# Optimization experiments

Measured on AMD Instinct MI355X. Metric: run time of the kernel, lower is better.

Reference implementation:

```python
import jax, jax.numpy as jnp
from jax import lax
import numpy as np
import math

B, L, UNITS, DM, P = 2048, 2, 16, 512, 16
CH = UNITS // P            # 1  (attention 'head' dim c)
D = DM // P                # 32
C_ATT = CH * D             # 32 channels in patch space
C_FFN = 4 * C_ATT          # 128
HALF = P // 2              # 8 (post-stride-2 patch size)
EPS = 1e-5


def _to_patches(x):
    # 'b (c p1) (d p2) -> b (c d) p1 p2'
    b = x.shape[0]
    x = x.reshape(b, CH, P, D, P).transpose(0, 1, 3, 2, 4)
    return x.reshape(b, CH * D, P, P)


def _from_patches(x):
    # 'b (c d) p1 p2 -> b (c p1) (d p2)'
    b = x.shape[0]
    x = x.reshape(b, CH, D, P, P).transpose(0, 1, 3, 2, 4)
    return x.reshape(b, CH * P, D * P)


def _layernorm(x, g, b):
    m = jnp.mean(x, -1, keepdims=True)
    v = jnp.mean((x - m) ** 2, -1, keepdims=True)
    return (x - m) * lax.rsqrt(v + EPS) * g + b


def _dw_block(x, dw_w, dw_b, bn_g, bn_b, bn_m, bn_v, pw_w, pw_b, stride):
    # depthwise 3x3 conv -> BatchNorm (eval) -> 1x1 pointwise conv
    C = x.shape[1]
    y = lax.conv_general_dilated(
        x, dw_w[:, None], (stride, stride), [(1, 1), (1, 1)],
        dimension_numbers=('NCHW', 'OIHW', 'NCHW'), feature_group_count=C)
    if dw_b is not None:
        y = y + dw_b[None, :, None, None]
    scale = (bn_g * lax.rsqrt(bn_v + EPS))[None, :, None, None]
    y = (y - bn_m[None, :, None, None]) * scale + bn_b[None, :, None, None]
    y = jnp.einsum('bchw,oc->bohw', y, pw_w)
    if pw_b is not None:
        y = y + pw_b[None, :, None, None]
    return y


def _encoder(x, ln1_g, ln1_b, ln2_g, ln2_b, qkv_dw, qkv_bng, qkv_bnb, qkv_bnm,
             qkv_bnv, qkv_pw, position, c1d_w, c1d_b, lin_w, lin_b,
             f1_w, f1_b, fdw_w, fdw_b, f_bng, f_bnb, f_bnm, f_bnv,
             fpw_w, fpw_b, f2_w, f2_b):
    b = x.shape[0]
    for l in range(L):
        # ---- attention sublayer (pre-norm) ----
        x1 = _layernorm(x, ln1_g[l], ln1_b[l])
        xp = _to_patches(x1)                              # (B, 32, 16, 16)
        qkv = [_dw_block(xp, qkv_dw[l, i], None,
                         qkv_bng[l, i], qkv_bnb[l, i], qkv_bnm[l, i], qkv_bnv[l, i],
                         qkv_pw[l, i], None, 2)           # (B, 32, 8, 8)
               .reshape(b, CH, D, HALF * HALF)            # 'b (c d) p1 p2 -> b c d (p1 p2)'
               for i in range(3)]
        q, k, v = qkv
        scores = jnp.einsum('bcde,bcfe->bcdf', q, k) / math.sqrt(HALF * HALF)
        scores = scores + position[l][None]               # (B, 1, 32, 32)
        p_attn = jax.nn.softmax(scores, axis=-1)
        o = jnp.einsum('bcdf,bcfe->bcde', p_attn, v)      # (B, 1, 32, 64)
        # 'b c d (p1 p2) -> b (c p1) (d p2)' with p1 = P//2
        o = o.reshape(b, CH, D, HALF, HALF).transpose(0, 1, 3, 2, 4)
        o = o.reshape(b, CH * HALF, D * HALF)             # (B, 8, 256)
        o = jnp.einsum('bcd,oc->bod', o, c1d_w[l]) + c1d_b[l][None, :, None]
        o = jnp.einsum('bcd,od->bco', o, lin_w[l]) + lin_b[l]  # (B, 16, 512)
        x = x + o
        # ---- conv-FFN sublayer ----
        x2 = _layernorm(x, ln2_g[l], ln2_b[l])
        y = _to_patches(x2)                               # (B, 32, 16, 16)
        y = jnp.einsum('bchw,oc->bohw', y, f1_w[l]) + f1_b[l][None, :, None, None]
        y = jax.nn.relu(y)                                # (B, 128, 16, 16)
        y = _dw_block(y, fdw_w[l], fdw_b[l], f_bng[l], f_bnb[l], f_bnm[l],
                      f_bnv[l], fpw_w[l], fpw_b[l], 1)
        y = jax.nn.relu(y)
        y = jnp.einsum('bchw,oc->bohw', y, f2_w[l]) + f2_b[l][None, :, None, None]
        x = x + _from_patches(y)
    return x


def setup_inputs():
    key = jax.random.key(0)
    ks = iter(jax.random.split(key, 16))
    nrm = lambda shape, s=0.05: jax.random.normal(next(ks), shape, jnp.float32) * s
    return dict(
        x=jax.random.normal(next(ks), (B, UNITS, DM), jnp.float32),
        ln1_g=jnp.ones((L, DM)), ln1_b=jnp.zeros((L, DM)),
        ln2_g=jnp.ones((L, DM)), ln2_b=jnp.zeros((L, DM)),
        qkv_dw=nrm((L, 3, C_ATT, 3, 3)),
        qkv_bng=jnp.ones((L, 3, C_ATT)), qkv_bnb=jnp.zeros((L, 3, C_ATT)),
        qkv_bnm=jnp.zeros((L, 3, C_ATT)), qkv_bnv=jnp.ones((L, 3, C_ATT)),
        qkv_pw=nrm((L, 3, C_ATT, C_ATT)),
        position=nrm((L, CH, D, D), 1.0),
        c1d_w=nrm((L, UNITS, UNITS // 2)), c1d_b=jnp.zeros((L, UNITS)),
        lin_w=nrm((L, DM, DM // 2)), lin_b=jnp.zeros((L, DM)),
        f1_w=nrm((L, C_FFN, C_ATT)), f1_b=jnp.zeros((L, C_FFN)),
        fdw_w=nrm((L, C_FFN, 3, 3)), fdw_b=jnp.zeros((L, C_FFN)),
        f_bng=jnp.ones((L, C_FFN)), f_bnb=jnp.zeros((L, C_FFN)),
        f_bnm=jnp.zeros((L, C_FFN)), f_bnv=jnp.ones((L, C_FFN)),
        fpw_w=nrm((L, C_FFN, C_FFN)), fpw_b=jnp.zeros((L, C_FFN)),
        f2_w=nrm((L, C_ATT, C_FFN)), f2_b=jnp.zeros((L, C_ATT)),
    )


def reference(x, ln1_g, ln1_b, ln2_g, ln2_b, qkv_dw, qkv_bng, qkv_bnb, qkv_bnm,
              qkv_bnv, qkv_pw, position, c1d_w, c1d_b, lin_w, lin_b,
              f1_w, f1_b, fdw_w, fdw_b, f_bng, f_bnb, f_bnm, f_bnv,
              fpw_w, fpw_b, f2_w, f2_b):
    return _encoder(x, ln1_g, ln1_b, ln2_g, ln2_b, qkv_dw, qkv_bng, qkv_bnb,
                    qkv_bnm, qkv_bnv, qkv_pw, position, c1d_w, c1d_b, lin_w,
                    lin_b, f1_w, f1_b, fdw_w, fdw_b, f_bng, f_bnb, f_bnm,
                    f_bnv, fpw_w, fpw_b, f2_w, f2_b)
```

## Files before the change

### kernel.cpp

```cpp
#include <hip/hip_runtime.h>
#include <hip/hip_bf16.h>

#define B_ 2048
#define EPSF 1e-5f

typedef __attribute__((ext_vector_type(8))) short short8v;
typedef __attribute__((ext_vector_type(4))) short short4v;
typedef __attribute__((ext_vector_type(4))) float f32x4;

__device__ __forceinline__ short f2bf_s(float f) {
  __hip_bfloat16 h = __float2bfloat16(f);
  return *reinterpret_cast<const short*>(&h);
}
__device__ __forceinline__ float bf2f(short s) {
  return __uint_as_float(((unsigned)(unsigned short)s) << 16);
}

__global__ __launch_bounds__(256) void k_prep(
    const float* __restrict__ f1_w, const float* __restrict__ fpw_w,
    const float* __restrict__ f2_w, const float* __restrict__ qkv_pw,
    const float* __restrict__ lin_w, const float* __restrict__ fdw_w,
    const float* __restrict__ fdw_b, const float* __restrict__ f_bng,
    const float* __restrict__ f_bnb, const float* __restrict__ f_bnm,
    const float* __restrict__ f_bnv, short* __restrict__ qkvA,
    short* __restrict__ linb, short* __restrict__ f1wb,
    short* __restrict__ img, float* __restrict__ convW,
    float* __restrict__ convB) {
  int i = blockIdx.x * 256 + threadIdx.x;
  if (i < 7680) {
    int l = i / 3840, r = i % 3840;
    int io = r / 40, c = r % 40;
    qkvA[i] = (c < 32) ? f2bf_s(qkv_pw[l * 3072 + io * 32 + c]) : (short)0;
  }
  if (i < 262144) linb[i] = f2bf_s(lin_w[i]);
  if (i < 10240) {
    int l = i / 5120, r = i % 5120, o = r / 40, kk = r % 40;
    f1wb[i] = (kk < 32) ? f2bf_s(f1_w[l * 4096 + o * 32 + kk]) : (short)0;
  }
  if (i < 48640) {
    int l = i / 24320, r = i % 24320;
    short val;
    if (r < 19456) {
      int o = r / 152, kk = r % 152;
      val = (kk < 128) ? f2bf_s(fpw_w[l * 16384 + o * 128 + kk]) : (short)0;
    } else {
      int r2 = r - 19456;
      int d = r2 / 152, kk = r2 % 152;
      val = (kk < 128) ? f2bf_s(f2_w[l * 4096 + d * 128 + kk]) : (short)0;
    }
    img[i] = val;
  }
  if (i < 256) {
    int l = i >> 7, c = i & 127;
    float scale = f_bng[l * 128 + c] * rsqrtf(f_bnv[l * 128 + c] + EPSF);
#pragma unroll
    for (int k = 0; k < 9; k++)
      convW[l * 1152 + k * 128 + c] = fdw_w[(l * 128 + c) * 9 + k] * scale;
    convB[l * 128 + c] =
        (fdw_b[l * 128 + c] - f_bnm[l * 128 + c]) * scale + f_bnb[l * 128 + c];
  }
}

__global__ __launch_bounds__(512) void k_att(
    const float* __restrict__ xin, const float* __restrict__ g,
    const float* __restrict__ beta, const float* __restrict__ dw,
    const float* __restrict__ bng, const float* __restrict__ bnb,
    const float* __restrict__ bnm, const float* __restrict__ bnv,
    const short* __restrict__ qkvA, const float* __restrict__ posn,
    const float* __restrict__ c1w, const float* __restrict__ c1b,
    const short* __restrict__ linb, const float* __restrict__ lin_b,
    float* __restrict__ xout) {
  __shared__ __align__(16) char smem[62592];
  float (*p)[257] = (float(*)[257])smem;
  float* sc  = (float*)(smem + 0);
  short* pa  = (short*)(smem + 4224);
  short* ore = (short*)(smem + 6784);
  short* xc1 = (short*)(smem + 11008);
  short* t3s = (short*)(smem + 32896);
  short* qe  = (short*)(smem + 48256);
  short* ke  = (short*)(smem + 52864);
  short* vt  = (short*)(smem + 57472);

  int b = blockIdx.x, tid = threadIdx.x;
  int lane = tid & 63, wid = tid >> 6;
  int row = lane & 15, kg = lane >> 4;
  const float* xb = xin + (size_t)b * 8192;
  float* xo = xout + (size_t)b * 8192;

  float xr[4][4];
#pragma unroll
  for (int t = 0; t < 4; t++)
#pragma unroll
    for (int r = 0; r < 4; r++)
      xr[t][r] = xb[(kg * 4 + r) * 512 + (wid * 4 + t) * 16 + row];

  for (int r = wid; r < 16; r += 8) {
    float vals[8];
    float s = 0.f, ss = 0.f;
#pragma unroll
    for (int j = 0; j < 8; j++) {
      float t = xb[r * 512 + lane + j * 64];
      vals[j] = t; s += t; ss += t * t;
    }
#pragma unroll
    for (int o = 32; o; o >>= 1) { s += __shfl_xor(s, o); ss += __shfl_xor(ss, o); }
    float m = s * (1.f / 512.f);
    float inv = rsqrtf(ss * (1.f / 512.f) - m * m + EPSF);
#pragma unroll
    for (int j = 0; j < 8; j++) {
      int col = lane + j * 64;
      p[col >> 4][r * 16 + (col & 15)] = (vals[j] - m) * inv * g[col] + beta[col];
    }
  }
  __syncthreads();

  {
    int c = tid & 31, oy = (tid >> 5) & 7, oxh = tid >> 8;
    int base = oxh * 8 - 1;
    float ra[9], rb[9], rc[9];
    int iy0 = 2 * oy - 1;
#pragma unroll
    for (int k = 0; k < 9; k++) {
      int ic = base + k;
      bool cv = (ic >= 0);
      ra[k] = (cv && iy0 >= 0) ? p[c][iy0 * 16 + ic] : 0.f;
      rb[k] = cv ? p[c][(2 * oy) * 16 + ic] : 0.f;
      rc[k] = cv ? p[c][(2 * oy + 1) * 16 + ic] : 0.f;
    }
    for (int iw = 0; iw < 3; iw++) {
      const float* w9 = dw + iw * 288 + c * 9;
      float w00 = w9[0], w01 = w9[1], w02 = w9[2];
      float w10 = w9[3], w11 = w9[4], w12 = w9[5];
      float w20 = w9[6], w21 = w9[7], w22 = w9[8];
      float scale = bng[iw * 32 + c] * rsqrtf(bnv[iw * 32 + c] + EPSF);
      float shift = bnb[iw * 32 + c] - bnm[iw * 32 + c] * scale;
#pragma unroll
      for (int j = 0; j < 4; j++) {
        int ox = oxh * 4 + j;
        float acc = w00 * ra[2 * j] + w01 * ra[2 * j + 1] + w02 * ra[2 * j + 2]
                  + w10 * rb[2 * j] + w11 * rb[2 * j + 1] + w12 * rb[2 * j + 2]
                  + w20 * rc[2 * j] + w21 * rc[2 * j + 1] + w22 * rc[2 * j + 2];
        t3s[(iw * 64 + oy * 8 + ox) * 40 + c] = f2bf_s(acc * scale + shift);
      }
    }
  }
  __syncthreads();

  {
    int mi = wid & 1, ni = wid >> 1;
    for (int iw = 0; iw < 3; iw++) {
      short8v a = *(const short8v*)&qkvA[(iw * 32 + mi * 16 + row) * 40 + kg * 8];
      short8v bb = *(const short8v*)&t3s[(iw * 64 + ni * 16 + row) * 40 + kg * 8];
      f32x4 z = {};
      f32x4 acc = __builtin_amdgcn_mfma_f32_16x16x32_bf16(a, bb, z, 0, 0, 0);
      if (iw < 2) {
        short* tgt = (iw == 0) ? qe : ke;
#pragma unroll
        for (int r = 0; r < 4; r++) {
          int d = mi * 16 + kg * 4 + r;
          tgt[d * 72 + ni * 16 + row] = f2bf_s(acc[r]);
        }
      } else {
        int e = ni * 16 + row;
        int fb = mi * 16 + kg * 4;
        short4v v0;
        v0.x = f2bf_s(acc[0]); v0.y = f2bf_s(acc[1]);
        v0.z = f2bf_s(acc[2]); v0.w = f2bf_s(acc[3]);
        *(short4v*)&vt[e * 40 + fb] = v0;
      }
    }
  }
  __syncthreads();

  if (wid < 4) {
    int mi = wid & 1, ni = (wid >> 1) & 1;
    f32x4 acc = {};
#pragma unroll
    for (int kk = 0; kk < 2; kk++) {
      short8v a = *(const short8v*)&qe[(mi * 16 + row) * 72 + kk * 32 + kg * 8];
      short8v bb = *(const short8v*)&ke[(ni * 16 + row) * 72 + kk * 32 + kg * 8];
      acc = __builtin_amdgcn_mfma_f32_16x16x32_bf16(a, bb, acc, 0, 0, 0);
    }
#pragma unroll
    for (int r = 0; r < 4; r++) {
      int d = mi * 16 + kg * 4 + r, f = ni * 16 + row;
      sc[d * 33 + f] = acc[r] * 0.125f + posn[d * 32 + f];
    }
  }
  __syncthreads();

  if (tid < 256) {
    int srow = tid >> 3, sg = tid & 7;
    float v0 = sc[srow * 33 + sg * 4 + 0];
    float v1 = sc[srow * 33 + sg * 4 + 1];
    float v2 = sc[srow * 33 + sg * 4 + 2];
    float v3 = sc[srow * 33 + sg * 4 + 3];
    float mx = fmaxf(fmaxf(v0, v1), fmaxf(v2, v3));
    mx = fmaxf(mx, __shfl_xor(mx, 1));
    mx = fmaxf(mx, __shfl_xor(mx, 2));
    mx = fmaxf(mx, __shfl_xor(mx, 4));
    float e0 = __expf(v0 - mx), e1 = __expf(v1 - mx);
    float e2 = __expf(v2 - mx), e3 = __expf(v3 - mx);
    float s = e0 + e1 + e2 + e3;
    s += __shfl_xor(s, 1); s += __shfl_xor(s, 2); s += __shfl_xor(s, 4);
    float inv = 1.f / s;
    short4v pk;
    pk.x = f2bf_s(e0 * inv); pk.y = f2bf_s(e1 * inv);
    pk.z = f2bf_s(e2 * inv); pk.w = f2bf_s(e3 * inv);
    *(short4v*)&pa[srow * 40 + sg * 4] = pk;
  }
  __syncthreads();

  {
    int mi = wid & 1, et = wid >> 1;
    short8v a = *(const short8v*)&pa[(mi * 16 + row) * 40 + kg * 8];
    int e = et * 16 + row;
    short8v bb = *(const short8v*)&vt[e * 40 + kg * 8];
    f32x4 z = {};
    f32x4 acc = __builtin_amdgcn_mfma_f32_16x16x32_bf16(a, bb, z, 0, 0, 0);
#pragma unroll
    for (int r = 0; r < 4; r++) {
      int d = mi * 16 + kg * 4 + r;
      ore[(e >> 3) * 264 + d * 8 + (e & 7)] = f2bf_s(acc[r]);
    }
  }
  __syncthreads();

  {
    int n = tid & 255, uh = tid >> 8;
    float o8[8];
#pragma unroll
    for (int c = 0; c < 8; c++) o8[c] = bf2f(ore[c * 264 + n]);
#pragma unroll
    for (int uu = 0; uu < 8; uu++) {
      int u = uh * 8 + uu;
      float acc = c1b[u];
#pragma unroll
      for (int c = 0; c < 8; c++) acc += c1w[u * 8 + c] * o8[c];
      xc1[u * 264 + n] = f2bf_s(acc);
    }
  }
  __syncthreads();

  {
    short8v a8[8];
#pragma unroll
    for (int kk = 0; kk < 8; kk++)
      a8[kk] = *(const short8v*)&xc1[row * 264 + kk * 32 + kg * 8];
#pragma unroll
    for (int t = 0; t < 4; t++) {
      int nt = wid * 4 + t;
      const short* bb_base = linb + (nt * 16 + row) * 256 + kg * 8;
      f32x4 acc = {};
#pragma unroll
      for (int kk = 0; kk < 8; kk++) {
        short8v bb = *(const short8v*)(bb_base + kk * 32);
        acc = __builtin_amdgcn_mfma_f32_16x16x32_bf16(a8[kk], bb, acc, 0, 0, 0);
      }
      int m = nt * 16 + row;
      float lb = lin_b[m];
#pragma unroll
      for (int r = 0; r < 4; r++) {
        int u = kg * 4 + r;
        xo[u * 512 + m] = xr[t][r] + acc[r] + lb;
      }
    }
  }
}

__global__ __launch_bounds__(1024, 4) void k_ffn4(
    const float* __restrict__ x, const float* __restrict__ g,
    const float* __restrict__ beta, const short* __restrict__ f1wg,
    const float* __restrict__ f1b, const float* __restrict__ convW,
    const float* __restrict__ convB, const short* __restrict__ img,
    const float* __restrict__ pwbias, const float* __restrict__ f2b,
    float* __restrict__ xg) {
  __shared__ __align__(16) char smem[149504];
  short* p_lds = (short*)smem;
  short* f1w_lds = (short*)(smem + 20480);
  short* sT = (short*)smem;
  short* sY = (short*)(smem + 77824);
  short* pw_lds = (short*)(smem + 77824);
  short* f2w_lds = (short*)(smem + 77824 + 38912);

  int b = blockIdx.x, tid = threadIdx.x;
  int lane = tid & 63, wid = tid >> 6;
  int row = lane & 15, kg = lane >> 4;
  const float* xb = x + (size_t)b * 8192;
  float* xo = xg + (size_t)b * 8192;

  const uint4* imgu = (const uint4*)img;
  uint4 pf0 = imgu[tid], pf1 = imgu[tid + 1024];
  uint4 pf2 = {};
  if (tid < 992) pf2 = imgu[tid + 2048];

  int cch = tid & 127;
  float w_[9];
#pragma unroll
  for (int k = 0; k < 9; k++) w_[k] = convW[k * 128 + cch];
  float cb = convB[cch];

  float xr[2][4];
#pragma unroll
  for (int mi = 0; mi < 2; mi++)
#pragma unroll
    for (int r2 = 0; r2 < 4; r2++)
      xr[mi][r2] = xo[wid * 512 + mi * 256 + kg * 64 + r2 * 16 + row];

  if (tid < 640) ((uint4*)f1w_lds)[tid] = ((const uint4*)f1wg)[tid];

  {
    int r = wid;
    float vals[8];
    float s = 0.f, ss = 0.f;
#pragma unroll
    for (int j = 0; j < 8; j++) {
      float t = xb[r * 512 + lane + j * 64];
      vals[j] = t; s += t; ss += t * t;
    }
#pragma unroll
    for (int o = 32; o; o >>= 1) { s += __shfl_xor(s, o); ss += __shfl_xor(ss, o); }
    float m = s * (1.f / 512.f);
    float inv = rsqrtf(ss * (1.f / 512.f) - m * m + EPSF);
#pragma unroll
    for (int j = 0; j < 8; j++) {
      int col = lane + j * 64;
      float nv = (vals[j] - m) * inv * g[col] + beta[col];
      p_lds[(r * 16 + (col & 15)) * 40 + (col >> 4)] = f2bf_s(nv);
    }
  }
  __syncthreads();

  {
    int o0 = (wid & 3) * 32, pos0 = (wid >> 2) * 64;
    short8v a0 = *(const short8v*)&f1w_lds[(o0 + row) * 40 + kg * 8];
    short8v a1 = *(const short8v*)&f1w_lds[(o0 + 16 + row) * 40 + kg * 8];
#pragma unroll
    for (int ni = 0; ni < 4; ni++) {
      short8v bb = *(const short8v*)&p_lds[(pos0 + ni * 16 + row) * 40 + kg * 8];
      f32x4 z = {};
      f32x4 c0 = __builtin_amdgcn_mfma_f32_16x16x32_bf16(a0, bb, z, 0, 0, 0);
      f32x4 c1 = __builtin_amdgcn_mfma_f32_16x16x32_bf16(a1, bb, z, 0, 0, 0);
      int pos = pos0 + ni * 16 + row;
#pragma unroll
      for (int r2 = 0; r2 < 4; r2++) {
        int c = o0 + kg * 4 + r2;
        sY[c * 280 + pos] = f2bf_s(fmaxf(c0[r2] + f1b[c], 0.f));
        sY[(c + 16) * 280 + pos] = f2bf_s(fmaxf(c1[r2] + f1b[c + 16], 0.f));
      }
    }
  }
  __syncthreads();

  {
    int c = cch, strip = tid >> 7;
#pragma unroll
    for (int j = 0; j < 2; j++) {
      int h = strip * 2 + j;
      float acc[16];
#pragma unroll
      for (int w = 0; w < 16; w++) acc[w] = cb;
#pragma unroll
      for (int rr = 0; rr < 3; rr++) {
        int rg = h - 1 + rr;
        if (rg < 0 || rg > 15) continue;
        short8v s0 = *(const short8v*)&sY[c * 280 + rg * 16];
        short8v s1 = *(const short8v*)&sY[c * 280 + rg * 16 + 8];
        float f[18];
        f[0] = 0.f; f[17] = 0.f;
#pragma unroll
        for (int i = 0; i < 8; i++) { f[1 + i] = bf2f(s0[i]); f[9 + i] = bf2f(s1[i]); }
        float w0 = w_[rr * 3], w1 = w_[rr * 3 + 1], w2 = w_[rr * 3 + 2];
#pragma unroll
        for (int w = 0; w < 16; w++)
          acc[w] += w0 * f[w] + w1 * f[w + 1] + w2 * f[w + 2];
      }
#pragma unroll
      for (int w = 0; w < 16; w++)
        sT[(h * 16 + w) * 152 + c] = f2bf_s(acc[w]);
    }
  }
  __syncthreads();

  {
    uint4* wdst = (uint4*)pw_lds;
    wdst[tid] = pf0; wdst[tid + 1024] = pf1;
    if (tid < 992) wdst[tid + 2048] = pf2;
  }
  __syncthreads();

  int o0 = (wid & 3) * 32, pos0 = (wid >> 2) * 64;
  f32x4 facc[2][4] = {};
#pragma unroll
  for (int kk = 0; kk < 4; kk++) {
    int k0 = kk * 32 + kg * 8;
    short8v a0 = *(const short8v*)&pw_lds[(o0 + row) * 152 + k0];
    short8v a1 = *(const short8v*)&pw_lds[(o0 + 16 + row) * 152 + k0];
    short8v bb[4];
#pragma unroll
    for (int ni = 0; ni < 4; ni++)
      bb[ni] = *(const short8v*)&sT[(pos0 + ni * 16 + row) * 152 + k0];
#pragma unroll
    for (int ni = 0; ni < 4; ni++) {
      facc[0][ni] = __builtin_amdgcn_mfma_f32_16x16x32_bf16(a0, bb[ni], facc[0][ni], 0, 0, 0);
      facc[1][ni] = __builtin_amdgcn_mfma_f32_16x16x32_bf16(a1, bb[ni], facc[1][ni], 0, 0, 0);
    }
  }
  __syncthreads();

#pragma unroll
  for (int mi = 0; mi < 2; mi++) {
    int ob = o0 + mi * 16 + kg * 4;
    float pb0 = pwbias[ob], pb1 = pwbias[ob + 1];
    float pb2 = pwbias[ob + 2], pb3 = pwbias[ob + 3];
#pragma unroll
    for (int ni = 0; ni < 4; ni++) {
      int pos = pos0 + ni * 16 + row;
      short4v pk;
      pk.x = f2bf_s(fmaxf(facc[mi][ni][0] + pb0, 0.f));
      pk.y = f2bf_s(fmaxf(facc[mi][ni][1] + pb1, 0.f));
      pk.z = f2bf_s(fmaxf(facc[mi][ni][2] + pb2, 0.f));
      pk.w = f2bf_s(fmaxf(facc[mi][ni][3] + pb3, 0.f));
      *(short4v*)&sT[pos * 152 + ob] = pk;
    }
  }
  __syncthreads();

  {
    f32x4 acc2[2] = {};
    int pos = wid * 16 + row;
#pragma unroll
    for (int kk = 0; kk < 4; kk++) {
      int k0 = kk * 32 + kg * 8;
      short8v a0 = *(const short8v*)&f2w_lds[row * 152 + k0];
      short8v a1 = *(const short8v*)&f2w_lds[(16 + row) * 152 + k0];
      short8v bb = *(const short8v*)&sT[pos * 152 + k0];
      acc2[0] = __builtin_amdgcn_mfma_f32_16x16x32_bf16(a0, bb, acc2[0], 0, 0, 0);
      acc2[1] = __builtin_amdgcn_mfma_f32_16x16x32_bf16(a1, bb, acc2[1], 0, 0, 0);
    }
#pragma unroll
    for (int mi = 0; mi < 2; mi++)
#pragma unroll
      for (int r2 = 0; r2 < 4; r2++) {
        int d = mi * 16 + kg * 4 + r2;
        xo[wid * 512 + mi * 256 + kg * 64 + r2 * 16 + row] =
            xr[mi][r2] + acc2[mi][r2] + f2b[d];
      }
  }
}

extern "C" void kernel_launch(void* const* d_in, const int* in_sizes, int n_in,
                              void* d_out, int out_size, void* d_ws, size_t ws_size,
                              hipStream_t stream) {
  const float* x_in   = (const float*)d_in[0];
  const float* ln1_g  = (const float*)d_in[1];
  const float* ln1_b  = (const float*)d_in[2];
  const float* ln2_g  = (const float*)d_in[3];
  const float* ln2_b  = (const float*)d_in[4];
  const float* qkv_dw = (const float*)d_in[5];
  const float* qkv_bng = (const float*)d_in[6];
  const float* qkv_bnb = (const float*)d_in[7];
  const float* qkv_bnm = (const float*)d_in[8];
  const float* qkv_bnv = (const float*)d_in[9];
  const float* qkv_pw = (const float*)d_in[10];
  const float* position = (const float*)d_in[11];
  const float* c1d_w  = (const float*)d_in[12];
  const float* c1d_b  = (const float*)d_in[13];
  const float* lin_w  = (const float*)d_in[14];
  const float* lin_b  = (const float*)d_in[15];
  const float* f1_w   = (const float*)d_in[16];
  const float* f1_b   = (const float*)d_in[17];
  const float* fdw_w  = (const float*)d_in[18];
  const float* fdw_b  = (const float*)d_in[19];
  const float* f_bng  = (const float*)d_in[20];
  const float* f_bnb  = (const float*)d_in[21];
  const float* f_bnm  = (const float*)d_in[22];
  const float* f_bnv  = (const float*)d_in[23];
  const float* fpw_w  = (const float*)d_in[24];
  const float* fpw_b  = (const float*)d_in[25];
  const float* f2_w   = (const float*)d_in[26];
  const float* f2_b   = (const float*)d_in[27];

  float* xbuf = (float*)d_out;
  short* qkvA = (short*)d_ws;
  short* linb = qkvA + 7680;
  short* f1wb = linb + 262144;
  short* img  = f1wb + 10240;
  float* convW = (float*)(img + 48640);
  float* convB = convW + 2304;

  k_prep<<<1024, 256, 0, stream>>>(f1_w, fpw_w, f2_w, qkv_pw, lin_w,
      fdw_w, fdw_b, f_bng, f_bnb, f_bnm, f_bnv,
      qkvA, linb, f1wb, img, convW, convB);
  for (int l = 0; l < 2; l++) {
    const float* xin = (l == 0) ? x_in : xbuf;
    k_att<<<B_, 512, 0, stream>>>(xin, ln1_g + l * 512, ln1_b + l * 512,
        qkv_dw + l * 864, qkv_bng + l * 96, qkv_bnb + l * 96,
        qkv_bnm + l * 96, qkv_bnv + l * 96, qkvA + l * 3840,
        position + l * 1024, c1d_w + l * 128, c1d_b + l * 16,
        linb + l * 131072, lin_b + l * 512, xbuf);
    k_ffn4<<<B_, 1024, 0, stream>>>(xbuf, ln2_g + l * 512, ln2_b + l * 512,
        f1wb + l * 5120, f1_b + l * 128, convW + l * 1152, convB + l * 128,
        img + l * 24320, fpw_b + l * 128, f2_b + l * 32, xbuf);
  }
}
```

Measured before the change: 383.8 us.

## Pack two samples per attention block with bf16 LDS and prefolded BN weights

The attention kernel now runs 1024 threads per block, each half handling one batch sample with its own LDS region. The layernormed patch buffer is stored in bf16 instead of fp32, which shrinks the per-sample LDS footprint so two samples fit in one block. The qkv depthwise weights are folded with BatchNorm once in the prep kernel and transposed for coalesced reads, and the qkv pointwise A fragments are preloaded into registers. The FFN kernel preloads its bias values into registers. The aims are better LDS/occupancy use and less redundant per-block weight work, at the cost of extra bf16 rounding on the conv input and more register pressure.

```diff
diff --git a/kernel.cpp b/kernel.cpp
--- a/kernel.cpp
+++ b/kernel.cpp
@@ -22,10 +22,13 @@
     const float* __restrict__ lin_w, const float* __restrict__ fdw_w,
     const float* __restrict__ fdw_b, const float* __restrict__ f_bng,
     const float* __restrict__ f_bnb, const float* __restrict__ f_bnm,
-    const float* __restrict__ f_bnv, short* __restrict__ qkvA,
-    short* __restrict__ linb, short* __restrict__ f1wb,
-    short* __restrict__ img, float* __restrict__ convW,
-    float* __restrict__ convB) {
+    const float* __restrict__ f_bnv, const float* __restrict__ qkv_dw,
+    const float* __restrict__ qkv_bng, const float* __restrict__ qkv_bnb,
+    const float* __restrict__ qkv_bnm, const float* __restrict__ qkv_bnv,
+    short* __restrict__ qkvA, short* __restrict__ linb,
+    short* __restrict__ f1wb, short* __restrict__ img,
+    float* __restrict__ convW, float* __restrict__ convB,
+    float* __restrict__ qkvdw, float* __restrict__ qkvdb) {
   int i = blockIdx.x * 256 + threadIdx.x;
   if (i < 7680) {
     int l = i / 3840, r = i % 3840;
@@ -59,31 +62,44 @@
     convB[l * 128 + c] =
         (fdw_b[l * 128 + c] - f_bnm[l * 128 + c]) * scale + f_bnb[l * 128 + c];
   }
+  if (i < 192) {
+    int l = i / 96, iw = (i % 96) / 32, c = i % 32;
+    int bi = l * 96 + iw * 32 + c;
+    float scale = qkv_bng[bi] * rsqrtf(qkv_bnv[bi] + EPSF);
+#pragma unroll
+    for (int k = 0; k < 9; k++)
+      qkvdw[((l * 3 + iw) * 9 + k) * 32 + c] =
+          qkv_dw[(l * 96 + iw * 32 + c) * 9 + k] * scale;
+    qkvdb[bi] = qkv_bnb[bi] - qkv_bnm[bi] * scale;
+  }
 }
 
-__global__ __launch_bounds__(512) void k_att(
+__global__ __launch_bounds__(1024, 4) void k_att2(
     const float* __restrict__ xin, const float* __restrict__ g,
-    const float* __restrict__ beta, const float* __restrict__ dw,
-    const float* __restrict__ bng, const float* __restrict__ bnb,
-    const float* __restrict__ bnm, const float* __restrict__ bnv,
-    const short* __restrict__ qkvA, const float* __restrict__ posn,
-    const float* __restrict__ c1w, const float* __restrict__ c1b,
-    const short* __restrict__ linb, const float* __restrict__ lin_b,
-    float* __restrict__ xout) {
-  __shared__ __align__(16) char smem[62592];
-  float (*p)[257] = (float(*)[257])smem;
-  float* sc  = (float*)(smem + 0);
-  short* pa  = (short*)(smem + 4224);
-  short* ore = (short*)(smem + 6784);
-  short* xc1 = (short*)(smem + 11008);
-  short* t3s = (short*)(smem + 32896);
-  short* qe  = (short*)(smem + 48256);
-  short* ke  = (short*)(smem + 52864);
-  short* vt  = (short*)(smem + 57472);
-
-  int b = blockIdx.x, tid = threadIdx.x;
+    const float* __restrict__ beta, const float* __restrict__ qkvdw,
+    const float* __restrict__ qkvdb, const short* __restrict__ qkvA,
+    const float* __restrict__ posn, const float* __restrict__ c1w,
+    const float* __restrict__ c1b, const short* __restrict__ linb,
+    const float* __restrict__ lin_b, float* __restrict__ xout) {
+  __shared__ __align__(16) char smem[93184];
+  int tid = threadIdx.x;
   int lane = tid & 63, wid = tid >> 6;
+  int s = wid >> 3, w8 = wid & 7;
   int row = lane & 15, kg = lane >> 4;
+  int tid511 = tid & 511;
+
+  char* sb = smem + s * 46592;
+  float* sc  = (float*)sb;
+  short* pbf = (short*)sb;
+  short* pa  = (short*)(sb + 4224);
+  short* ore = (short*)(sb + 6784);
+  short* t3s = (short*)(sb + 16896);
+  short* xc1 = (short*)(sb + 16896);
+  short* qe  = (short*)(sb + 32256);
+  short* ke  = (short*)(sb + 36864);
+  short* vt  = (short*)(sb + 41472);
+
+  int b = blockIdx.x * 2 + s;
   const float* xb = xin + (size_t)b * 8192;
   float* xo = xout + (size_t)b * 8192;
 
@@ -92,30 +108,36 @@
   for (int t = 0; t < 4; t++)
 #pragma unroll
     for (int r = 0; r < 4; r++)
-      xr[t][r] = xb[(kg * 4 + r) * 512 + (wid * 4 + t) * 16 + row];
-
-  for (int r = wid; r < 16; r += 8) {
+      xr[t][r] = xb[(kg * 4 + r) * 512 + (w8 * 4 + t) * 16 + row];
+  int mi_pw = w8 & 1;
+  short8v aq[3];
+#pragma unroll
+  for (int iw = 0; iw < 3; iw++)
+    aq[iw] = *(const short8v*)&qkvA[(iw * 32 + mi_pw * 16 + row) * 40 + kg * 8];
+
+  for (int r = w8; r < 16; r += 8) {
     float vals[8];
-    float s = 0.f, ss = 0.f;
+    float sm = 0.f, ss = 0.f;
 #pragma unroll
     for (int j = 0; j < 8; j++) {
       float t = xb[r * 512 + lane + j * 64];
-      vals[j] = t; s += t; ss += t * t;
-    }
-#pragma unroll
-    for (int o = 32; o; o >>= 1) { s += __shfl_xor(s, o); ss += __shfl_xor(ss, o); }
-    float m = s * (1.f / 512.f);
+      vals[j] = t; sm += t; ss += t * t;
+    }
+#pragma unroll
+    for (int o = 32; o; o >>= 1) { sm += __shfl_xor(sm, o); ss += __shfl_xor(ss, o); }
+    float m = sm * (1.f / 512.f);
     float inv = rsqrtf(ss * (1.f / 512.f) - m * m + EPSF);
 #pragma unroll
     for (int j = 0; j < 8; j++) {
       int col = lane + j * 64;
-      p[col >> 4][r * 16 + (col & 15)] = (vals[j] - m) * inv * g[col] + beta[col];
-    }
-  }
-  __syncthreads();
-
-  {
-    int c = tid & 31, oy = (tid >> 5) & 7, oxh = tid >> 8;
+      float nv = (vals[j] - m) * inv * g[col] + beta[col];
+      pbf[(col >> 4) * 264 + r * 16 + (col & 15)] = f2bf_s(nv);
+    }
+  }
+  __syncthreads();
+
+  {
+    int c = tid511 & 31, oy = (tid511 >> 5) & 7, oxh = tid511 >> 8;
     int base = oxh * 8 - 1;
     float ra[9], rb[9], rc[9];
     int iy0 = 2 * oy - 1;
@@ -123,36 +145,34 @@
     for (int k = 0; k < 9; k++) {
       int ic = base + k;
       bool cv = (ic >= 0);
-      ra[k] = (cv && iy0 >= 0) ? p[c][iy0 * 16 + ic] : 0.f;
-      rb[k] = cv ? p[c][(2 * oy) * 16 + ic] : 0.f;
-      rc[k] = cv ? p[c][(2 * oy + 1) * 16 + ic] : 0.f;
+      ra[k] = (cv && iy0 >= 0) ? bf2f(pbf[c * 264 + iy0 * 16 + ic]) : 0.f;
+      rb[k] = cv ? bf2f(pbf[c * 264 + (2 * oy) * 16 + ic]) : 0.f;
+      rc[k] = cv ? bf2f(pbf[c * 264 + (2 * oy + 1) * 16 + ic]) : 0.f;
     }
     for (int iw = 0; iw < 3; iw++) {
-      const float* w9 = dw + iw * 288 + c * 9;
-      float w00 = w9[0], w01 = w9[1], w02 = w9[2];
-      float w10 = w9[3], w11 = w9[4], w12 = w9[5];
-      float w20 = w9[6], w21 = w9[7], w22 = w9[8];
-      float scale = bng[iw * 32 + c] * rsqrtf(bnv[iw * 32 + c] + EPSF);
-      float shift = bnb[iw * 32 + c] - bnm[iw * 32 + c] * scale;
+      const float* w9 = qkvdw + iw * 288;
+      float w00 = w9[0 * 32 + c], w01 = w9[1 * 32 + c], w02 = w9[2 * 32 + c];
+      float w10 = w9[3 * 32 + c], w11 = w9[4 * 32 + c], w12 = w9[5 * 32 + c];
+      float w20 = w9[6 * 32 + c], w21 = w9[7 * 32 + c], w22 = w9[8 * 32 + c];
+      float shift = qkvdb[iw * 32 + c];
 #pragma unroll
       for (int j = 0; j < 4; j++) {
         int ox = oxh * 4 + j;
         float acc = w00 * ra[2 * j] + w01 * ra[2 * j + 1] + w02 * ra[2 * j + 2]
                   + w10 * rb[2 * j] + w11 * rb[2 * j + 1] + w12 * rb[2 * j + 2]
                   + w20 * rc[2 * j] + w21 * rc[2 * j + 1] + w22 * rc[2 * j + 2];
-        t3s[(iw * 64 + oy * 8 + ox) * 40 + c] = f2bf_s(acc * scale + shift);
-      }
-    }
-  }
-  __syncthreads();
-
-  {
-    int mi = wid & 1, ni = wid >> 1;
+        t3s[(iw * 64 + oy * 8 + ox) * 40 + c] = f2bf_s(acc + shift);
+      }
+    }
+  }
+  __syncthreads();
+
+  {
+    int mi = mi_pw, ni = w8 >> 1;
     for (int iw = 0; iw < 3; iw++) {
-      short8v a = *(const short8v*)&qkvA[(iw * 32 + mi * 16 + row) * 40 + kg * 8];
       short8v bb = *(const short8v*)&t3s[(iw * 64 + ni * 16 + row) * 40 + kg * 8];
       f32x4 z = {};
-      f32x4 acc = __builtin_amdgcn_mfma_f32_16x16x32_bf16(a, bb, z, 0, 0, 0);
+      f32x4 acc = __builtin_amdgcn_mfma_f32_16x16x32_bf16(aq[iw], bb, z, 0, 0, 0);
       if (iw < 2) {
         short* tgt = (iw == 0) ? qe : ke;
 #pragma unroll
@@ -172,8 +192,8 @@
   }
   __syncthreads();
 
-  if (wid < 4) {
-    int mi = wid & 1, ni = (wid >> 1) & 1;
+  if (w8 < 4) {
+    int mi = w8 & 1, ni = (w8 >> 1) & 1;
     f32x4 acc = {};
 #pragma unroll
     for (int kk = 0; kk < 2; kk++) {
@@ -189,8 +209,8 @@
   }
   __syncthreads();
 
-  if (tid < 256) {
-    int srow = tid >> 3, sg = tid & 7;
+  if (tid511 < 256) {
+    int srow = tid511 >> 3, sg = tid511 & 7;
     float v0 = sc[srow * 33 + sg * 4 + 0];
     float v1 = sc[srow * 33 + sg * 4 + 1];
     float v2 = sc[srow * 33 + sg * 4 + 2];
@@ -201,9 +221,9 @@
     mx = fmaxf(mx, __shfl_xor(mx, 4));
     float e0 = __expf(v0 - mx), e1 = __expf(v1 - mx);
     float e2 = __expf(v2 - mx), e3 = __expf(v3 - mx);
-    float s = e0 + e1 + e2 + e3;
-    s += __shfl_xor(s, 1); s += __shfl_xor(s, 2); s += __shfl_xor(s, 4);
-    float inv = 1.f / s;
+    float sum = e0 + e1 + e2 + e3;
+    sum += __shfl_xor(sum, 1); sum += __shfl_xor(sum, 2); sum += __shfl_xor(sum, 4);
+    float inv = 1.f / sum;
     short4v pk;
     pk.x = f2bf_s(e0 * inv); pk.y = f2bf_s(e1 * inv);
     pk.z = f2bf_s(e2 * inv); pk.w = f2bf_s(e3 * inv);
@@ -212,7 +232,7 @@
   __syncthreads();
 
   {
-    int mi = wid & 1, et = wid >> 1;
+    int mi = w8 & 1, et = w8 >> 1;
     short8v a = *(const short8v*)&pa[(mi * 16 + row) * 40 + kg * 8];
     int e = et * 16 + row;
     short8v bb = *(const short8v*)&vt[e * 40 + kg * 8];
@@ -227,7 +247,7 @@
   __syncthreads();
 
   {
-    int n = tid & 255, uh = tid >> 8;
+    int n = tid511 & 255, uh = tid511 >> 8;
     float o8[8];
 #pragma unroll
     for (int c = 0; c < 8; c++) o8[c] = bf2f(ore[c * 264 + n]);
@@ -249,7 +269,7 @@
       a8[kk] = *(const short8v*)&xc1[row * 264 + kk * 32 + kg * 8];
 #pragma unroll
     for (int t = 0; t < 4; t++) {
-      int nt = wid * 4 + t;
+      int nt = w8 * 4 + t;
       const short* bb_base = linb + (nt * 16 + row) * 256 + kg * 8;
       f32x4 acc = {};
 #pragma unroll
@@ -299,6 +319,17 @@
 #pragma unroll
   for (int k = 0; k < 9; k++) w_[k] = convW[k * 128 + cch];
   float cb = convB[cch];
+  int o0 = (wid & 3) * 32;
+  float f1bv[8], pwbv[8], f2bv[8];
+#pragma unroll
+  for (int j = 0; j < 4; j++) {
+    f1bv[j]     = f1b[o0 + kg * 4 + j];
+    f1bv[4 + j] = f1b[o0 + 16 + kg * 4 + j];
+    pwbv[j]     = pwbias[o0 + kg * 4 + j];
+    pwbv[4 + j] = pwbias[o0 + 16 + kg * 4 + j];
+    f2bv[j]     = f2b[kg * 4 + j];
+    f2bv[4 + j] = f2b[16 + kg * 4 + j];
+  }
 
   float xr[2][4];
 #pragma unroll
@@ -332,7 +363,7 @@
   __syncthreads();
 
   {
-    int o0 = (wid & 3) * 32, pos0 = (wid >> 2) * 64;
+    int pos0 = (wid >> 2) * 64;
     short8v a0 = *(const short8v*)&f1w_lds[(o0 + row) * 40 + kg * 8];
     short8v a1 = *(const short8v*)&f1w_lds[(o0 + 16 + row) * 40 + kg * 8];
 #pragma unroll
@@ -345,8 +376,8 @@
 #pragma unroll
       for (int r2 = 0; r2 < 4; r2++) {
         int c = o0 + kg * 4 + r2;
-        sY[c * 280 + pos] = f2bf_s(fmaxf(c0[r2] + f1b[c], 0.f));
-        sY[(c + 16) * 280 + pos] = f2bf_s(fmaxf(c1[r2] + f1b[c + 16], 0.f));
+        sY[c * 280 + pos] = f2bf_s(fmaxf(c0[r2] + f1bv[r2], 0.f));
+        sY[(c + 16) * 280 + pos] = f2bf_s(fmaxf(c1[r2] + f1bv[4 + r2], 0.f));
       }
     }
   }
@@ -389,7 +420,7 @@
   }
   __syncthreads();
 
-  int o0 = (wid & 3) * 32, pos0 = (wid >> 2) * 64;
+  int pos0 = (wid >> 2) * 64;
   f32x4 facc[2][4] = {};
 #pragma unroll
   for (int kk = 0; kk < 4; kk++) {
@@ -411,16 +442,14 @@
 #pragma unroll
   for (int mi = 0; mi < 2; mi++) {
     int ob = o0 + mi * 16 + kg * 4;
-    float pb0 = pwbias[ob], pb1 = pwbias[ob + 1];
-    float pb2 = pwbias[ob + 2], pb3 = pwbias[ob + 3];
 #pragma unroll
     for (int ni = 0; ni < 4; ni++) {
       int pos = pos0 + ni * 16 + row;
       short4v pk;
-      pk.x = f2bf_s(fmaxf(facc[mi][ni][0] + pb0, 0.f));
-      pk.y = f2bf_s(fmaxf(facc[mi][ni][1] + pb1, 0.f));
-      pk.z = f2bf_s(fmaxf(facc[mi][ni][2] + pb2, 0.f));
-      pk.w = f2bf_s(fmaxf(facc[mi][ni][3] + pb3, 0.f));
+      pk.x = f2bf_s(fmaxf(facc[mi][ni][0] + pwbv[mi * 4 + 0], 0.f));
+      pk.y = f2bf_s(fmaxf(facc[mi][ni][1] + pwbv[mi * 4 + 1], 0.f));
+      pk.z = f2bf_s(fmaxf(facc[mi][ni][2] + pwbv[mi * 4 + 2], 0.f));
+      pk.w = f2bf_s(fmaxf(facc[mi][ni][3] + pwbv[mi * 4 + 3], 0.f));
       *(short4v*)&sT[pos * 152 + ob] = pk;
     }
   }
@@ -442,9 +471,8 @@
     for (int mi = 0; mi < 2; mi++)
 #pragma unroll
       for (int r2 = 0; r2 < 4; r2++) {
-        int d = mi * 16 + kg * 4 + r2;
         xo[wid * 512 + mi * 256 + kg * 64 + r2 * 16 + row] =
-            xr[mi][r2] + acc2[mi][r2] + f2b[d];
+            xr[mi][r2] + acc2[mi][r2] + f2bv[mi * 4 + r2];
       }
   }
 }
@@ -488,15 +516,17 @@
   short* img  = f1wb + 10240;
   float* convW = (float*)(img + 48640);
   float* convB = convW + 2304;
+  float* qkvdw = convB + 256;
+  float* qkvdb = qkvdw + 1728;
 
   k_prep<<<1024, 256, 0, stream>>>(f1_w, fpw_w, f2_w, qkv_pw, lin_w,
       fdw_w, fdw_b, f_bng, f_bnb, f_bnm, f_bnv,
-      qkvA, linb, f1wb, img, convW, convB);
+      qkv_dw, qkv_bng, qkv_bnb, qkv_bnm, qkv_bnv,
+      qkvA, linb, f1wb, img, convW, convB, qkvdw, qkvdb);
   for (int l = 0; l < 2; l++) {
     const float* xin = (l == 0) ? x_in : xbuf;
-    k_att<<<B_, 512, 0, stream>>>(xin, ln1_g + l * 512, ln1_b + l * 512,
-        qkv_dw + l * 864, qkv_bng + l * 96, qkv_bnb + l * 96,
-        qkv_bnm + l * 96, qkv_bnv + l * 96, qkvA + l * 3840,
+    k_att2<<<B_ / 2, 1024, 0, stream>>>(xin, ln1_g + l * 512, ln1_b + l * 512,
+        qkvdw + l * 864, qkvdb + l * 96, qkvA + l * 3840,
         position + l * 1024, c1d_w + l * 128, c1d_b + l * 16,
         linb + l * 131072, lin_b + l * 512, xbuf);
     k_ffn4<<<B_, 1024, 0, stream>>>(xbuf, ln2_g + l * 512, ln2_b + l * 512,
```

Measured after the change: 410.2 us. 6.9% more time.
